# Kernel tuning notes

Hardware: AMD Instinct MI355X
Metric: run time of the kernel (lower is better)

Reference implementation:

```python
import jax, jax.numpy as jnp
import numpy as np


def setup_inputs() -> dict:
    key = jax.random.key(0)
    ks = jax.random.split(key, 9)
    B, T, D, U = 512, 1024, 64, 128
    inp = {
        'inputs': jax.random.normal(ks[0], (B, T, D), dtype=jnp.float32),
        'W_f': jax.random.normal(ks[1], (D, U), dtype=jnp.float32) * 0.05,
        'U_f': jax.random.normal(ks[2], (U, U), dtype=jnp.float32) * 0.05,
        'b_f': jnp.zeros((U,), dtype=jnp.float32),
        'W_i': jax.random.normal(ks[3], (D, U), dtype=jnp.float32) * 0.05,
        'U_i': jax.random.normal(ks[4], (U, U), dtype=jnp.float32) * 0.05,
        'b_i': jnp.zeros((U,), dtype=jnp.float32),
        'W_c': jax.random.normal(ks[5], (D, U), dtype=jnp.float32) * 0.05,
        'U_c': jax.random.normal(ks[6], (U, U), dtype=jnp.float32) * 0.05,
        'b_c': jnp.zeros((U,), dtype=jnp.float32),
        'W_o': jax.random.normal(ks[7], (D, U), dtype=jnp.float32) * 0.05,
        'U_o': jax.random.normal(ks[8], (U, U), dtype=jnp.float32) * 0.05,
        'b_o': jnp.zeros((U,), dtype=jnp.float32),
    }
    return inp


def _lstm(inputs, W_f, U_f, b_f, W_i, U_i, b_i, W_c, U_c, b_c, W_o, U_o, b_o):
    B, T, D = inputs.shape
    U = W_f.shape[1]
    # Precompute all input-to-gate projections in one batched GEMM per gate: [B,T,U]
    xf = jnp.einsum('btd,du->btu', inputs, W_f) + b_f
    xi = jnp.einsum('btd,du->btu', inputs, W_i) + b_i
    xc = jnp.einsum('btd,du->btu', inputs, W_c) + b_c
    xo = jnp.einsum('btd,du->btu', inputs, W_o) + b_o
    # time-major stacked gate inputs: [T, B, 4, U]
    xg = jnp.stack([xf, xi, xc, xo], axis=2).transpose(1, 0, 2, 3)
    # concatenated recurrent weights: [U, 4U]
    U_all = jnp.concatenate([U_f, U_i, U_c, U_o], axis=1)

    def step(carry, x_t):
        h, c = carry
        # x_t: [B, 4, U]
        rec = (h @ U_all).reshape(B, 4, U)
        g = x_t + rec
        f = jax.nn.sigmoid(g[:, 0])
        i = jax.nn.sigmoid(g[:, 1])
        c_tilde = jnp.tanh(g[:, 2])
        o = jax.nn.sigmoid(g[:, 3])
        c_new = f * c + i * c_tilde
        h_new = o * jnp.tanh(c_new)
        return (h_new, c_new), None

    h0 = jnp.zeros((B, U), dtype=inputs.dtype)
    c0 = jnp.zeros((B, U), dtype=inputs.dtype)
    (h, c), _ = jax.lax.scan(step, (h0, c0), xg)
    return h


def reference(inputs, W_f, U_f, b_f, W_i, U_i, b_i, W_c, U_c, b_c, W_o, U_o, b_o):
    return _lstm(inputs, W_f, U_f, b_f, W_i, U_i, b_i, W_c, U_c, b_c, W_o, U_o, b_o)
```

## Files before the change

### kernel.cpp

```cpp
#include <hip/hip_runtime.h>
#include <stdint.h>


typedef __attribute__((ext_vector_type(8))) short short8;
typedef __attribute__((ext_vector_type(4))) float floatx4;
typedef __attribute__((ext_vector_type(4))) int   intx4;
typedef __attribute__((ext_vector_type(8))) int   intx8;

#define B_SZ   512
#define T_SZ   1024
#define D_SZ   64
#define U_SZ   128
#define ROWS   2
#define NBLK   (B_SZ / ROWS)
#define NTHR   512
#define A1STRB 160
#define GXSTR  524

__device__ __forceinline__ short f2bf(float f) {
    uint32_t u = __builtin_bit_cast(uint32_t, f);
    uint32_t r = (u + 0x7fffu + ((u >> 16) & 1u)) >> 16;
    return (short)r;
}
__device__ __forceinline__ int cvt2bf(float lo, float hi) {
    int r;
    asm("v_cvt_pk_bf16_f32 %0, %1, %2" : "=v"(r) : "v"(lo), "v"(hi));
    return r;
}
__device__ __forceinline__ short8 pk8(float4 a, float4 b) {
    intx4 t = {cvt2bf(a.x, a.y), cvt2bf(a.z, a.w), cvt2bf(b.x, b.y), cvt2bf(b.z, b.w)};
    return __builtin_bit_cast(short8, t);
}
__device__ __forceinline__ float fsig(float x) {
    return __builtin_amdgcn_rcpf(1.0f + __builtin_amdgcn_exp2f(-1.4426950408889634f * x));
}
__device__ __forceinline__ float ftanh(float x) {
    return 1.0f - 2.0f * __builtin_amdgcn_rcpf(1.0f + __builtin_amdgcn_exp2f(2.8853900817779268f * x));
}
__device__ __forceinline__ void sync_lds() {
    asm volatile("s_waitcnt lgkmcnt(0)\n\ts_barrier" ::: "memory");
}

__global__ __launch_bounds__(NTHR, 2) void lstm_persistent(
    const float* __restrict__ xin,
    const float* __restrict__ Wf, const float* __restrict__ Uf, const float* __restrict__ bfp,
    const float* __restrict__ Wi, const float* __restrict__ Ui, const float* __restrict__ bip,
    const float* __restrict__ Wc, const float* __restrict__ Uc, const float* __restrict__ bcp,
    const float* __restrict__ Wo, const float* __restrict__ Uo, const float* __restrict__ bop,
    float* __restrict__ out)
{
    __shared__ float Gx[2][16 * GXSTR];
    __shared__ __align__(8) char A1[2][2 * A1STRB];

    const int tid  = threadIdx.x;
    const int wave = tid >> 6;
    const int lane = tid & 63;
    const int quad = lane >> 4;
    const int nlo  = lane & 15;
    const int blk  = blockIdx.x;

    const float* Wg[4] = {Wf, Wi, Wc, Wo};
    const float* Ug[4] = {Uf, Ui, Uc, Uo};
    const float* Bg[4] = {bfp, bip, bcp, bop};

    if (wave < 4) {
        __builtin_amdgcn_s_setprio(1);
        const int ti_s = quad & 1;
        const int prow = quad >> 1;
        const int u_s  = 32 * wave + 16 * ti_s + nlo;

        intx8 bU8[4][2];
#pragma unroll
        for (int g = 0; g < 4; ++g)
#pragma unroll
            for (int ti = 0; ti < 2; ++ti) {
                const int uc = 32 * wave + 16 * ti + nlo;
#pragma unroll
                for (int d = 0; d < 8; ++d) {
                    const int k0 = quad * 32 + d * 4;
                    int pk = __builtin_amdgcn_cvt_pk_fp8_f32(
                        Ug[g][(k0 + 0) * U_SZ + uc], Ug[g][(k0 + 1) * U_SZ + uc], 0, 0);
                    pk = __builtin_amdgcn_cvt_pk_fp8_f32(
                        Ug[g][(k0 + 2) * U_SZ + uc], Ug[g][(k0 + 3) * U_SZ + uc], pk, 1);
                    bU8[g][ti][d] = pk;
                }
            }
        float c_st = 0.0f;

        for (int i = tid; i < 2 * 2 * A1STRB; i += 256) ((char*)A1)[i] = 0;
        __syncthreads();

        for (int g = 0; g < 128; ++g) {
            const float* GxR = &Gx[g & 1][0];
#pragma unroll
            for (int j = 0; j < 8; ++j) {
                const char* ap = &A1[j & 1][(nlo >> 3) * A1STRB + quad * 32];
                intx4 alo = *(const intx4*)(ap);
                intx4 ahi = *(const intx4*)(ap + 16);
                floatx4 gx = *(const floatx4*)&GxR[(2 * j + prow) * GXSTR + 4 * u_s];
                intx8 a8 = {alo.x, alo.y, alo.z, alo.w, ahi.x, ahi.y, ahi.z, ahi.w};

                floatx4 acc0[4], acc1[4];
#pragma unroll
                for (int gt = 0; gt < 4; ++gt) {
                    floatx4 z = (floatx4){0.f, 0.f, 0.f, 0.f};
                    acc0[gt] = __builtin_amdgcn_mfma_scale_f32_16x16x128_f8f6f4(
                        a8, bU8[gt][0], z, 0, 0, 0, 0x7f7f7f7f, 0, 0x7f7f7f7f);
                }
#pragma unroll
                for (int gt = 0; gt < 4; ++gt) {
                    floatx4 z = (floatx4){0.f, 0.f, 0.f, 0.f};
                    acc1[gt] = __builtin_amdgcn_mfma_scale_f32_16x16x128_f8f6f4(
                        a8, bU8[gt][1], z, 0, 0, 0, 0x7f7f7f7f, 0, 0x7f7f7f7f);
                }

                float g0 = (ti_s ? acc1[0][0] : acc0[0][0]) + gx[0];
                float g1 = (ti_s ? acc1[1][0] : acc0[1][0]) + gx[1];
                float g2 = (ti_s ? acc1[2][0] : acc0[2][0]) + gx[2];
                float g3 = (ti_s ? acc1[3][0] : acc0[3][0]) + gx[3];
                float fg = fsig(g0), ig = fsig(g1), ctl = ftanh(g2), og = fsig(g3);
                float c = fg * c_st + ig * ctl;
                float h = og * ftanh(c);
                c_st = c;

                if (g == 127 && j == 7) {
                    out[(size_t)(blk * ROWS + prow) * U_SZ + u_s] = h;
                } else {
                    int pk = __builtin_amdgcn_cvt_pk_fp8_f32(h, h, 0, 0);
                    A1[(j & 1) ^ 1][prow * A1STRB + u_s] = (char)(pk & 0xff);
                }
                sync_lds();
            }
        }
    } else {
        const int p = wave - 4;
        const int brow  = nlo & 1;
        const int t_off = nlo >> 1;

        short8 bWp[8][2];
        float  bw[8];
#pragma unroll
        for (int tau = 0; tau < 8; ++tau) {
            const int gt = tau >> 1;
            const int uc = 16 * (2 * p + (tau & 1)) + nlo;
            bw[tau] = Bg[gt][uc];
#pragma unroll
            for (int kt = 0; kt < 2; ++kt)
#pragma unroll
                for (int jj = 0; jj < 8; ++jj) {
                    int k = kt * 32 + quad * 8 + jj;
                    bWp[tau][kt][jj] = f2bf(Wg[gt][k * U_SZ + uc]);
                }
        }

        const float* xg = xin + ((size_t)(blk * ROWS + brow) * T_SZ) * D_SZ + quad * 8;

        float4 p0 = *(const float4*)(xg + (size_t)t_off * D_SZ + 0);
        float4 p1 = *(const float4*)(xg + (size_t)t_off * D_SZ + 4);
        float4 p2 = *(const float4*)(xg + (size_t)t_off * D_SZ + 32);
        float4 p3 = *(const float4*)(xg + (size_t)t_off * D_SZ + 36);
        float4 q0 = *(const float4*)(xg + (size_t)(8 + t_off) * D_SZ + 0);
        float4 q1 = *(const float4*)(xg + (size_t)(8 + t_off) * D_SZ + 4);
        float4 q2 = *(const float4*)(xg + (size_t)(8 + t_off) * D_SZ + 32);
        float4 q3 = *(const float4*)(xg + (size_t)(8 + t_off) * D_SZ + 36);

        short8 xa0 = pk8(p0, p1);
        short8 xa1 = pk8(p2, p3);
#pragma unroll
        for (int tau = 0; tau < 8; ++tau) {
            const int gt = tau >> 1;
            const int uc = 16 * (2 * p + (tau & 1)) + nlo;
            floatx4 acc = (floatx4){0.f, 0.f, 0.f, 0.f};
            acc = __builtin_amdgcn_mfma_f32_16x16x32_bf16(xa0, bWp[tau][0], acc, 0, 0, 0);
            acc = __builtin_amdgcn_mfma_f32_16x16x32_bf16(xa1, bWp[tau][1], acc, 0, 0, 0);
#pragma unroll
            for (int r = 0; r < 4; ++r)
                Gx[0][(quad * 4 + r) * GXSTR + 4 * uc + gt] = acc[r] + bw[tau];
        }
        xa0 = pk8(q0, q1);
        xa1 = pk8(q2, q3);
        float4 xq0 = *(const float4*)(xg + (size_t)(16 + t_off) * D_SZ + 0);
        float4 xq1 = *(const float4*)(xg + (size_t)(16 + t_off) * D_SZ + 4);
        float4 xq2 = *(const float4*)(xg + (size_t)(16 + t_off) * D_SZ + 32);
        float4 xq3 = *(const float4*)(xg + (size_t)(16 + t_off) * D_SZ + 36);
        __syncthreads();

        short8 xn0 = xa0, xn1 = xa1;
        for (int g = 0; g < 128; ++g) {
            float* GxW = &Gx[(g + 1) & 1][0];
#pragma unroll
            for (int j = 0; j < 8; ++j) {
                if (j == 0 && g <= 125) {
                    xn0 = pk8(xq0, xq1);
                    xn1 = pk8(xq2, xq3);
                }
                if (j == 1 && g <= 124) {
                    const float* b = xg + (size_t)(8 * (g + 3) + t_off) * D_SZ;
                    xq0 = *(const float4*)(b + 0);
                    xq1 = *(const float4*)(b + 4);
                    xq2 = *(const float4*)(b + 32);
                    xq3 = *(const float4*)(b + 36);
                }
                if (g < 127) {
                    const int uc = 16 * (2 * p + (j & 1)) + nlo;
                    floatx4 acc = (floatx4){0.f, 0.f, 0.f, 0.f};
                    acc = __builtin_amdgcn_mfma_f32_16x16x32_bf16(xa0, bWp[j][0], acc, 0, 0, 0);
                    acc = __builtin_amdgcn_mfma_f32_16x16x32_bf16(xa1, bWp[j][1], acc, 0, 0, 0);
#pragma unroll
                    for (int r = 0; r < 4; ++r)
                        GxW[(quad * 4 + r) * GXSTR + 4 * uc + (j >> 1)] = acc[r] + bw[j];
                }
                sync_lds();
            }
            xa0 = xn0; xa1 = xn1;
        }
    }
}

extern "C" void kernel_launch(void* const* d_in, const int* in_sizes, int n_in,
                              void* d_out, int out_size, void* d_ws, size_t ws_size,
                              hipStream_t stream) {
    (void)in_sizes; (void)n_in; (void)d_ws; (void)ws_size; (void)out_size;
    const float* xin = (const float*)d_in[0];
    const float* Wf  = (const float*)d_in[1];
    const float* Uf  = (const float*)d_in[2];
    const float* bf  = (const float*)d_in[3];
    const float* Wi  = (const float*)d_in[4];
    const float* Ui  = (const float*)d_in[5];
    const float* bi  = (const float*)d_in[6];
    const float* Wc  = (const float*)d_in[7];
    const float* Uc  = (const float*)d_in[8];
    const float* bc  = (const float*)d_in[9];
    const float* Wo  = (const float*)d_in[10];
    const float* Uo  = (const float*)d_in[11];
    const float* bo  = (const float*)d_in[12];
    float* out = (float*)d_out;

    hipLaunchKernelGGL(lstm_persistent, dim3(NBLK), dim3(NTHR), 0, stream,
                       xin, Wf, Uf, bf, Wi, Ui, bi, Wc, Uc, bc, Wo, Uo, bo, out);
}
```

Before: 545.6 us.

## Unify warp roles so all eight waves do recurrence and input projection

Replaces the producer/consumer split (four waves running the recurrent MFMA, four precomputing input projections) with a uniform scheme. Each of the eight waves owns 16 hidden units, runs four fp8 MFMAs per step instead of eight, and interleaves the bf16 input-projection MFMAs on odd substeps. The exp2 scaling constants are folded into the stored Gx values so the gate nonlinearities start from a single FMA. The aim is to shorten the serial per-step critical path. In exchange, half the lanes now compute redundant gate values and the projection work sits inline on the recurrence waves.

```diff
diff --git a/kernel.cpp b/kernel.cpp
--- a/kernel.cpp
+++ b/kernel.cpp
@@ -16,6 +16,7 @@
 #define NTHR   512
 #define A1STRB 160
 #define GXSTR  524
+#define L2E    1.4426950408889634f
 
 __device__ __forceinline__ short f2bf(float f) {
     uint32_t u = __builtin_bit_cast(uint32_t, f);
@@ -31,11 +32,14 @@
     intx4 t = {cvt2bf(a.x, a.y), cvt2bf(a.z, a.w), cvt2bf(b.x, b.y), cvt2bf(b.z, b.w)};
     return __builtin_bit_cast(short8, t);
 }
-__device__ __forceinline__ float fsig(float x) {
-    return __builtin_amdgcn_rcpf(1.0f + __builtin_amdgcn_exp2f(-1.4426950408889634f * x));
+__device__ __forceinline__ float fsig2(float e) {
+    return __builtin_amdgcn_rcpf(1.0f + __builtin_amdgcn_exp2f(e));
+}
+__device__ __forceinline__ float fth2(float e) {
+    return 1.0f - 2.0f * __builtin_amdgcn_rcpf(1.0f + __builtin_amdgcn_exp2f(e));
 }
 __device__ __forceinline__ float ftanh(float x) {
-    return 1.0f - 2.0f * __builtin_amdgcn_rcpf(1.0f + __builtin_amdgcn_exp2f(2.8853900817779268f * x));
+    return 1.0f - 2.0f * __builtin_amdgcn_rcpf(1.0f + __builtin_amdgcn_exp2f(2.0f * L2E * x));
 }
 __device__ __forceinline__ void sync_lds() {
     asm volatile("s_waitcnt lgkmcnt(0)\n\ts_barrier" ::: "memory");
@@ -62,158 +66,134 @@
     const float* Wg[4] = {Wf, Wi, Wc, Wo};
     const float* Ug[4] = {Uf, Ui, Uc, Uo};
     const float* Bg[4] = {bfp, bip, bcp, bop};
-
-    if (wave < 4) {
-        __builtin_amdgcn_s_setprio(1);
-        const int ti_s = quad & 1;
-        const int prow = quad >> 1;
-        const int u_s  = 32 * wave + 16 * ti_s + nlo;
-
-        intx8 bU8[4][2];
-#pragma unroll
-        for (int g = 0; g < 4; ++g)
-#pragma unroll
-            for (int ti = 0; ti < 2; ++ti) {
-                const int uc = 32 * wave + 16 * ti + nlo;
-#pragma unroll
-                for (int d = 0; d < 8; ++d) {
-                    const int k0 = quad * 32 + d * 4;
-                    int pk = __builtin_amdgcn_cvt_pk_fp8_f32(
-                        Ug[g][(k0 + 0) * U_SZ + uc], Ug[g][(k0 + 1) * U_SZ + uc], 0, 0);
-                    pk = __builtin_amdgcn_cvt_pk_fp8_f32(
-                        Ug[g][(k0 + 2) * U_SZ + uc], Ug[g][(k0 + 3) * U_SZ + uc], pk, 1);
-                    bU8[g][ti][d] = pk;
-                }
-            }
-        float c_st = 0.0f;
-
-        for (int i = tid; i < 2 * 2 * A1STRB; i += 256) ((char*)A1)[i] = 0;
-        __syncthreads();
-
-        for (int g = 0; g < 128; ++g) {
-            const float* GxR = &Gx[g & 1][0];
-#pragma unroll
-            for (int j = 0; j < 8; ++j) {
-                const char* ap = &A1[j & 1][(nlo >> 3) * A1STRB + quad * 32];
-                intx4 alo = *(const intx4*)(ap);
-                intx4 ahi = *(const intx4*)(ap + 16);
-                floatx4 gx = *(const floatx4*)&GxR[(2 * j + prow) * GXSTR + 4 * u_s];
-                intx8 a8 = {alo.x, alo.y, alo.z, alo.w, ahi.x, ahi.y, ahi.z, ahi.w};
-
-                floatx4 acc0[4], acc1[4];
-#pragma unroll
-                for (int gt = 0; gt < 4; ++gt) {
-                    floatx4 z = (floatx4){0.f, 0.f, 0.f, 0.f};
-                    acc0[gt] = __builtin_amdgcn_mfma_scale_f32_16x16x128_f8f6f4(
-                        a8, bU8[gt][0], z, 0, 0, 0, 0x7f7f7f7f, 0, 0x7f7f7f7f);
-                }
-#pragma unroll
-                for (int gt = 0; gt < 4; ++gt) {
-                    floatx4 z = (floatx4){0.f, 0.f, 0.f, 0.f};
-                    acc1[gt] = __builtin_amdgcn_mfma_scale_f32_16x16x128_f8f6f4(
-                        a8, bU8[gt][1], z, 0, 0, 0, 0x7f7f7f7f, 0, 0x7f7f7f7f);
-                }
-
-                float g0 = (ti_s ? acc1[0][0] : acc0[0][0]) + gx[0];
-                float g1 = (ti_s ? acc1[1][0] : acc0[1][0]) + gx[1];
-                float g2 = (ti_s ? acc1[2][0] : acc0[2][0]) + gx[2];
-                float g3 = (ti_s ? acc1[3][0] : acc0[3][0]) + gx[3];
-                float fg = fsig(g0), ig = fsig(g1), ctl = ftanh(g2), og = fsig(g3);
-                float c = fg * c_st + ig * ctl;
-                float h = og * ftanh(c);
-                c_st = c;
-
-                if (g == 127 && j == 7) {
-                    out[(size_t)(blk * ROWS + prow) * U_SZ + u_s] = h;
-                } else {
-                    int pk = __builtin_amdgcn_cvt_pk_fp8_f32(h, h, 0, 0);
-                    A1[(j & 1) ^ 1][prow * A1STRB + u_s] = (char)(pk & 0xff);
-                }
-                sync_lds();
-            }
+    const float scg[4] = {-L2E, -L2E, 2.0f * L2E, -L2E};
+
+    const int  u_s  = 16 * wave + nlo;
+    const int  prow = quad >> 1;
+    const bool wr   = (quad & 1) == 0;
+
+    intx8 bU8[4];
+#pragma unroll
+    for (int gt = 0; gt < 4; ++gt)
+#pragma unroll
+        for (int d = 0; d < 8; ++d) {
+            const int k0 = quad * 32 + d * 4;
+            int pk = __builtin_amdgcn_cvt_pk_fp8_f32(
+                Ug[gt][(k0 + 0) * U_SZ + u_s], Ug[gt][(k0 + 1) * U_SZ + u_s], 0, 0);
+            pk = __builtin_amdgcn_cvt_pk_fp8_f32(
+                Ug[gt][(k0 + 2) * U_SZ + u_s], Ug[gt][(k0 + 3) * U_SZ + u_s], pk, 1);
+            bU8[gt][d] = pk;
         }
-    } else {
-        const int p = wave - 4;
-        const int brow  = nlo & 1;
-        const int t_off = nlo >> 1;
-
-        short8 bWp[8][2];
-        float  bw[8];
-#pragma unroll
-        for (int tau = 0; tau < 8; ++tau) {
-            const int gt = tau >> 1;
-            const int uc = 16 * (2 * p + (tau & 1)) + nlo;
-            bw[tau] = Bg[gt][uc];
-#pragma unroll
-            for (int kt = 0; kt < 2; ++kt)
-#pragma unroll
-                for (int jj = 0; jj < 8; ++jj) {
-                    int k = kt * 32 + quad * 8 + jj;
-                    bWp[tau][kt][jj] = f2bf(Wg[gt][k * U_SZ + uc]);
-                }
+
+    short8 bWp[4][2];
+    float  bw[4];
+#pragma unroll
+    for (int gt = 0; gt < 4; ++gt) {
+        bw[gt] = Bg[gt][u_s];
+#pragma unroll
+        for (int kt = 0; kt < 2; ++kt)
+#pragma unroll
+            for (int jj = 0; jj < 8; ++jj) {
+                int k = kt * 32 + quad * 8 + jj;
+                bWp[gt][kt][jj] = f2bf(Wg[gt][k * U_SZ + u_s]);
+            }
+    }
+
+    for (int i = tid; i < 2 * 2 * A1STRB; i += NTHR) ((char*)A1)[i] = 0;
+
+    const int brow  = nlo & 1;
+    const int t_off = nlo >> 1;
+    const float* xg = xin + ((size_t)(blk * ROWS + brow) * T_SZ) * D_SZ + quad * 8;
+
+    float4 p0 = *(const float4*)(xg + (size_t)t_off * D_SZ + 0);
+    float4 p1 = *(const float4*)(xg + (size_t)t_off * D_SZ + 4);
+    float4 p2 = *(const float4*)(xg + (size_t)t_off * D_SZ + 32);
+    float4 p3 = *(const float4*)(xg + (size_t)t_off * D_SZ + 36);
+    float4 q0 = *(const float4*)(xg + (size_t)(8 + t_off) * D_SZ + 0);
+    float4 q1 = *(const float4*)(xg + (size_t)(8 + t_off) * D_SZ + 4);
+    float4 q2 = *(const float4*)(xg + (size_t)(8 + t_off) * D_SZ + 32);
+    float4 q3 = *(const float4*)(xg + (size_t)(8 + t_off) * D_SZ + 36);
+
+    short8 xa0 = pk8(p0, p1);
+    short8 xa1 = pk8(p2, p3);
+#pragma unroll
+    for (int gt = 0; gt < 4; ++gt) {
+        floatx4 acc = (floatx4){0.f, 0.f, 0.f, 0.f};
+        acc = __builtin_amdgcn_mfma_f32_16x16x32_bf16(xa0, bWp[gt][0], acc, 0, 0, 0);
+        acc = __builtin_amdgcn_mfma_f32_16x16x32_bf16(xa1, bWp[gt][1], acc, 0, 0, 0);
+#pragma unroll
+        for (int r = 0; r < 4; ++r)
+            Gx[0][(quad * 4 + r) * GXSTR + 4 * u_s + gt] = (acc[r] + bw[gt]) * scg[gt];
+    }
+    xa0 = pk8(q0, q1);
+    xa1 = pk8(q2, q3);
+    float4 xq0 = *(const float4*)(xg + (size_t)(16 + t_off) * D_SZ + 0);
+    float4 xq1 = *(const float4*)(xg + (size_t)(16 + t_off) * D_SZ + 4);
+    float4 xq2 = *(const float4*)(xg + (size_t)(16 + t_off) * D_SZ + 32);
+    float4 xq3 = *(const float4*)(xg + (size_t)(16 + t_off) * D_SZ + 36);
+    __syncthreads();
+
+    float  c_st = 0.0f;
+    short8 xn0 = xa0, xn1 = xa1;
+    for (int g = 0; g < 128; ++g) {
+        const float* GxR = &Gx[g & 1][0];
+        float*       GxW = &Gx[(g + 1) & 1][0];
+#pragma unroll
+        for (int j = 0; j < 8; ++j) {
+            __builtin_amdgcn_s_setprio(1);
+            const char* ap = &A1[j & 1][(nlo >> 3) * A1STRB + quad * 32];
+            intx4 alo = *(const intx4*)(ap);
+            intx4 ahi = *(const intx4*)(ap + 16);
+            floatx4 gx = *(const floatx4*)&GxR[(2 * j + prow) * GXSTR + 4 * u_s];
+            intx8 a8 = {alo.x, alo.y, alo.z, alo.w, ahi.x, ahi.y, ahi.z, ahi.w};
+
+            floatx4 acc[4];
+#pragma unroll
+            for (int gt = 0; gt < 4; ++gt) {
+                floatx4 z = (floatx4){0.f, 0.f, 0.f, 0.f};
+                acc[gt] = __builtin_amdgcn_mfma_scale_f32_16x16x128_f8f6f4(
+                    a8, bU8[gt], z, 0, 0, 0, 0x7f7f7f7f, 0, 0x7f7f7f7f);
+            }
+
+            float fg = fsig2(__builtin_fmaf(acc[0][0], -L2E, gx[0]));
+            float ig = fsig2(__builtin_fmaf(acc[1][0], -L2E, gx[1]));
+            float ct = fth2 (__builtin_fmaf(acc[2][0], 2.0f * L2E, gx[2]));
+            float og = fsig2(__builtin_fmaf(acc[3][0], -L2E, gx[3]));
+            float c  = fg * c_st + ig * ct;
+            float h  = og * ftanh(c);
+            c_st = c;
+
+            if (g == 127 && j == 7) {
+                if (wr) out[(size_t)(blk * ROWS + prow) * U_SZ + u_s] = h;
+            } else if (wr) {
+                int pk = __builtin_amdgcn_cvt_pk_fp8_f32(h, h, 0, 0);
+                A1[(j & 1) ^ 1][prow * A1STRB + u_s] = (char)(pk & 0xff);
+            }
+            __builtin_amdgcn_s_setprio(0);
+
+            if (j == 0 && g <= 125) {
+                xn0 = pk8(xq0, xq1);
+                xn1 = pk8(xq2, xq3);
+            }
+            if (j == 2 && g <= 124) {
+                const float* b = xg + (size_t)(8 * (g + 3) + t_off) * D_SZ;
+                xq0 = *(const float4*)(b + 0);
+                xq1 = *(const float4*)(b + 4);
+                xq2 = *(const float4*)(b + 32);
+                xq3 = *(const float4*)(b + 36);
+            }
+            if ((j & 1) && g < 127) {
+                const int gt = j >> 1;
+                floatx4 acc2 = (floatx4){0.f, 0.f, 0.f, 0.f};
+                acc2 = __builtin_amdgcn_mfma_f32_16x16x32_bf16(xa0, bWp[gt][0], acc2, 0, 0, 0);
+                acc2 = __builtin_amdgcn_mfma_f32_16x16x32_bf16(xa1, bWp[gt][1], acc2, 0, 0, 0);
+#pragma unroll
+                for (int r = 0; r < 4; ++r)
+                    GxW[(quad * 4 + r) * GXSTR + 4 * u_s + gt] = (acc2[r] + bw[gt]) * scg[gt];
+            }
+            sync_lds();
         }
-
-        const float* xg = xin + ((size_t)(blk * ROWS + brow) * T_SZ) * D_SZ + quad * 8;
-
-        float4 p0 = *(const float4*)(xg + (size_t)t_off * D_SZ + 0);
-        float4 p1 = *(const float4*)(xg + (size_t)t_off * D_SZ + 4);
-        float4 p2 = *(const float4*)(xg + (size_t)t_off * D_SZ + 32);
-        float4 p3 = *(const float4*)(xg + (size_t)t_off * D_SZ + 36);
-        float4 q0 = *(const float4*)(xg + (size_t)(8 + t_off) * D_SZ + 0);
-        float4 q1 = *(const float4*)(xg + (size_t)(8 + t_off) * D_SZ + 4);
-        float4 q2 = *(const float4*)(xg + (size_t)(8 + t_off) * D_SZ + 32);
-        float4 q3 = *(const float4*)(xg + (size_t)(8 + t_off) * D_SZ + 36);
-
-        short8 xa0 = pk8(p0, p1);
-        short8 xa1 = pk8(p2, p3);
-#pragma unroll
-        for (int tau = 0; tau < 8; ++tau) {
-            const int gt = tau >> 1;
-            const int uc = 16 * (2 * p + (tau & 1)) + nlo;
-            floatx4 acc = (floatx4){0.f, 0.f, 0.f, 0.f};
-            acc = __builtin_amdgcn_mfma_f32_16x16x32_bf16(xa0, bWp[tau][0], acc, 0, 0, 0);
-            acc = __builtin_amdgcn_mfma_f32_16x16x32_bf16(xa1, bWp[tau][1], acc, 0, 0, 0);
-#pragma unroll
-            for (int r = 0; r < 4; ++r)
-                Gx[0][(quad * 4 + r) * GXSTR + 4 * uc + gt] = acc[r] + bw[tau];
-        }
-        xa0 = pk8(q0, q1);
-        xa1 = pk8(q2, q3);
-        float4 xq0 = *(const float4*)(xg + (size_t)(16 + t_off) * D_SZ + 0);
-        float4 xq1 = *(const float4*)(xg + (size_t)(16 + t_off) * D_SZ + 4);
-        float4 xq2 = *(const float4*)(xg + (size_t)(16 + t_off) * D_SZ + 32);
-        float4 xq3 = *(const float4*)(xg + (size_t)(16 + t_off) * D_SZ + 36);
-        __syncthreads();
-
-        short8 xn0 = xa0, xn1 = xa1;
-        for (int g = 0; g < 128; ++g) {
-            float* GxW = &Gx[(g + 1) & 1][0];
-#pragma unroll
-            for (int j = 0; j < 8; ++j) {
-                if (j == 0 && g <= 125) {
-                    xn0 = pk8(xq0, xq1);
-                    xn1 = pk8(xq2, xq3);
-                }
-                if (j == 1 && g <= 124) {
-                    const float* b = xg + (size_t)(8 * (g + 3) + t_off) * D_SZ;
-                    xq0 = *(const float4*)(b + 0);
-                    xq1 = *(const float4*)(b + 4);
-                    xq2 = *(const float4*)(b + 32);
-                    xq3 = *(const float4*)(b + 36);
-                }
-                if (g < 127) {
-                    const int uc = 16 * (2 * p + (j & 1)) + nlo;
-                    floatx4 acc = (floatx4){0.f, 0.f, 0.f, 0.f};
-                    acc = __builtin_amdgcn_mfma_f32_16x16x32_bf16(xa0, bWp[j][0], acc, 0, 0, 0);
-                    acc = __builtin_amdgcn_mfma_f32_16x16x32_bf16(xa1, bWp[j][1], acc, 0, 0, 0);
-#pragma unroll
-                    for (int r = 0; r < 4; ++r)
-                        GxW[(quad * 4 + r) * GXSTR + 4 * uc + (j >> 1)] = acc[r] + bw[j];
-                }
-                sync_lds();
-            }
-            xa0 = xn0; xa1 = xn1;
-        }
+        xa0 = xn0; xa1 = xn1;
     }
 }
 
```

New measurement: 577.0 us. 1.06x slower.
